# Optimization experiments

Measured on AMD Instinct MI355X. Metric: run time of the kernel, lower is better.

Reference implementation:

```python
import jax, jax.numpy as jnp
import numpy as np

K = 3
STRIDE = 1
PAD = 1
DIL = 1


def _unfold(a):
    # a: (N, C, H, W) -> patches (N, C, K*K, oH, oW), matching torch.F.unfold
    # channel-major ordering (c slowest, then kernel row, then kernel col).
    N, C, H, W = a.shape
    oH = (H + 2 * PAD - DIL * (K - 1) - 1) // STRIDE + 1
    oW = (W + 2 * PAD - DIL * (K - 1) - 1) // STRIDE + 1
    ap = jnp.pad(a, ((0, 0), (0, 0), (PAD, PAD), (PAD, PAD)))
    cols = []
    for i in range(K):
        for j in range(K):
            cols.append(ap[:, :,
                           i * DIL: i * DIL + (oH - 1) * STRIDE + 1: STRIDE,
                           j * DIL: j * DIL + (oW - 1) * STRIDE + 1: STRIDE])
    return jnp.stack(cols, axis=2)  # (N, C, K*K, oH, oW)


def setup_inputs() -> dict:
    key = jax.random.key(0)
    k1, k2, k3, k4, k5 = jax.random.split(key, 5)
    N, C, O, H, W = 4, 128, 256, 128, 128
    x = jax.random.normal(k1, (N, C, H, W), dtype=jnp.float32)
    depth = jax.random.uniform(k2, (N, 1, H, W), dtype=jnp.float32)
    camera_params = jax.random.normal(k3, (N, 4), dtype=jnp.float32)
    weight = jax.random.normal(k4, (O, C, K, K), dtype=jnp.float32) * 0.05
    bias = jax.random.normal(k5, (O,), dtype=jnp.float32) * 0.05
    return {"x": x, "depth": depth, "camera_params": camera_params,
            "weight": weight, "bias": bias}


def reference(x, depth, camera_params, weight, bias):
    # camera_params is accepted but unused, mirroring the torch module.
    O, C = weight.shape[0], weight.shape[1]
    xp = _unfold(x)        # (N, C, kk, oH, oW)
    dp = _unfold(depth)    # (N, 1, kk, oH, oW)
    w = weight.reshape(O, C, K * K)
    # depth-modulated im2col GEMM: sum_{c,p} w[o,c,p] * x_patch * d_patch
    out = jnp.einsum('ocp,ncpxy->noxy', w, xp * dp)
    return out + bias[None, :, None, None]
```

## Files before the change

kernel.cpp:

```cpp
#include <hip/hip_runtime.h>
#include <stdint.h>


#define C_IN 128
#define O_OUT 256
#define HW 128
#define NB 4
#define PADW 130

#define XD_ELEMS ((size_t)NB * PADW * PADW * C_IN)
#define XD_BYTES (XD_ELEMS * 2)
#define WT_ELEMS ((size_t)O_OUT * C_IN * 9)
#define WT_BYTES (WT_ELEMS * 2)

typedef __attribute__((ext_vector_type(8))) short short8;
typedef __attribute__((ext_vector_type(4))) float f32x4;
typedef __attribute__((ext_vector_type(4))) unsigned uint4v;

__device__ __forceinline__ unsigned f2bf_bits(float f) {
  unsigned u = __builtin_bit_cast(unsigned, f);
  return (u + 0x7fffu + ((u >> 16) & 1u)) >> 16;
}

__device__ __forceinline__ void async_load16(const void* g, void* l) {
  __builtin_amdgcn_global_load_lds(
      (__attribute__((address_space(1))) void*)g,
      (__attribute__((address_space(3))) void*)l, 16, 0, 0);
}

__global__ __launch_bounds__(256) void prep_xd(const float* __restrict__ x,
                                               const float* __restrict__ depth,
                                               short* __restrict__ xd) {
  __shared__ short s[128 * 130];

  const int R = blockIdx.x;
  if (R >= NB * HW) {
    const int n = R - NB * HW;
    uint4v* base0 = (uint4v*)(xd + (size_t)n * PADW * PADW * C_IN);
    uint4v* base1 = (uint4v*)(xd + ((size_t)n * PADW + (PADW - 1)) * PADW * C_IN);
    const uint4v z = {0u, 0u, 0u, 0u};
    const int per_row = PADW * C_IN * 2 / 16;
    for (int i = threadIdx.x; i < per_row; i += 256) {
      base0[i] = z;
      base1[i] = z;
    }
    return;
  }

  const int n = R >> 7, y = R & 127;
  const int tid = threadIdx.x;
  const int lane = tid & 63;
  const int wave = tid >> 6;

  {
    unsigned* row = (unsigned*)(xd + ((size_t)(n * PADW + y + 1) * PADW) * C_IN);
    if (tid < 64) row[tid] = 0u;
    else if (tid < 128) row[(size_t)(PADW - 1) * 64 + (tid - 64)] = 0u;
  }

  typedef __attribute__((ext_vector_type(2))) float f32x2;
  const f32x2 d2 = *(const f32x2*)(depth + ((size_t)n * HW + y) * HW + 2 * lane);
  const float* xrow = x + (((size_t)n * C_IN) * HW + y) * HW + 2 * lane;
#pragma unroll 8
  for (int ci = 0; ci < 32; ++ci) {
    const int c = ci * 4 + wave;
    const f32x2 v = *(const f32x2*)(xrow + (size_t)c * HW * HW);
    s[(2 * lane) * 130 + c] = (short)f2bf_bits(v.x * d2.x);
    s[(2 * lane + 1) * 130 + c] = (short)f2bf_bits(v.y * d2.y);
  }
  __syncthreads();

  unsigned* orow = (unsigned*)(xd + ((size_t)(n * PADW + y + 1) * PADW + 1) * C_IN);
#pragma unroll 8
  for (int i = 0; i < 32; ++i) {
    const int flat = tid + i * 256;
    const int px = flat >> 6, cp = flat & 63;
    orow[flat] = ((const unsigned*)s)[px * 65 + cp];
  }
}

__global__ void prep_wt(const float* __restrict__ w, short* __restrict__ wt) {
  const int gid = blockIdx.x * 256 + threadIdx.x;
  if (gid >= (int)WT_ELEMS) return;
  const int c = gid & 127;
  const int tap = (gid >> 7) % 9;
  const int o = gid / (9 * 128);
  wt[gid] = (short)f2bf_bits(w[((size_t)o * C_IN + c) * 9 + tap]);
}

__global__ __launch_bounds__(256, 2) void conv_mfma(
    const short* __restrict__ xd, const short* __restrict__ wt,
    const float* __restrict__ bias, float* __restrict__ out) {
  __shared__ short lds[24576];

  const int tid = threadIdx.x;
  const int bx = blockIdx.x;
  const int n = bx >> 6;
  const int y = (bx & 63) << 1;
  const int o0 = blockIdx.y << 7;
  const int lane = tid & 63;
  const int wave = tid >> 6;
  const int wm = wave & 1, wn = wave >> 1;
  const int ln = lane & 15, q = lane >> 4;

  const int row0 = tid >> 2;
  const int part = tid & 3;

  const short* wg0 = wt + (size_t)(o0 + row0) * 1152 + part * 8;
  const short* wg1 = wg0 + (size_t)64 * 1152;
  const short* xh0 = xd + ((size_t)(n * PADW + y) * PADW + row0) * C_IN + part * 8;
  const short* xh1 = xh0 + (size_t)PADW * C_IN;

  f32x4 acc[4][8] = {};

  auto stage = [&](int kt) {
    const int tap = kt >> 2;
    const int cc = kt & 3;
    const int ti = tap / 3;
    const int tj = tap - ti * 3;
    const int wo = kt << 5;
    const int xo = (ti * PADW + tj) * C_IN + (cc << 5);
    short* lb = lds + ((kt & 1) ? 12288 : 0) + tid * 8;
    async_load16(wg0 + wo, lb);
    async_load16(wg1 + wo, lb + 2048);
    async_load16(xh0 + xo, lb + 4096);
    async_load16(xh0 + 64 * C_IN + xo, lb + 6144);
    async_load16(xh1 + xo, lb + 8192);
    async_load16(xh1 + 64 * C_IN + xo, lb + 10240);
  };

  stage(0);

#pragma unroll 4
  for (int kt = 0; kt < 36; ++kt) {
    __syncthreads();

    if (kt + 1 < 36) stage(kt + 1);

    const short* Ws = lds + ((kt & 1) ? 12288 : 0);
    const short* Xs = Ws + 4096;

    short8 a[4], b[8];
#pragma unroll
    for (int t = 0; t < 4; ++t)
      a[t] = *(const short8*)(Ws + (((wm << 6) + (t << 4) + ln) << 5) + (q << 3));
#pragma unroll
    for (int u = 0; u < 8; ++u)
      b[u] = *(const short8*)(Xs + (((wn << 7) + (u << 4) + ln) << 5) + (q << 3));
#pragma unroll
    for (int t = 0; t < 4; ++t)
#pragma unroll
      for (int u = 0; u < 8; ++u)
        acc[t][u] =
            __builtin_amdgcn_mfma_f32_16x16x32_bf16(a[t], b[u], acc[t][u], 0, 0, 0);
  }

#pragma unroll
  for (int t = 0; t < 4; ++t) {
    const int ob = o0 + (wm << 6) + (t << 4) + (q << 2);
#pragma unroll
    for (int u = 0; u < 8; ++u) {
      const int xcol = (u << 4) + ln;
      const int yrow = y + wn;
#pragma unroll
      for (int r = 0; r < 4; ++r) {
        const int o = ob + r;
        out[(((size_t)n * O_OUT + o) * HW + yrow) * HW + xcol] =
            acc[t][u][r] + bias[o];
      }
    }
  }
}

__global__ void conv_naive(const float* __restrict__ x,
                           const float* __restrict__ depth,
                           const float* __restrict__ w,
                           const float* __restrict__ bias,
                           float* __restrict__ out) {
  const int gid = blockIdx.x * 256 + threadIdx.x;
  if (gid >= NB * O_OUT * HW * HW) return;
  const int xc = gid & 127;
  const int y = (gid >> 7) & 127;
  const int o = (gid >> 14) & 255;
  const int n = gid >> 22;
  float s = bias[o];
  for (int c = 0; c < C_IN; ++c)
    for (int i = 0; i < 3; ++i) {
      const int yy = y + i - 1;
      if (yy < 0 || yy >= HW) continue;
      for (int j = 0; j < 3; ++j) {
        const int xx = xc + j - 1;
        if (xx < 0 || xx >= HW) continue;
        s += w[((o * C_IN + c) * 3 + i) * 3 + j] *
             x[(((size_t)n * C_IN + c) * HW + yy) * HW + xx] *
             depth[((size_t)n * HW + yy) * HW + xx];
      }
    }
  out[gid] = s;
}

extern "C" void kernel_launch(void* const* d_in, const int* in_sizes, int n_in,
                              void* d_out, int out_size, void* d_ws, size_t ws_size,
                              hipStream_t stream) {
  const float* x = (const float*)d_in[0];
  const float* depth = (const float*)d_in[1];
  const float* weight = (const float*)d_in[3];
  const float* bias = (const float*)d_in[4];
  float* out = (float*)d_out;

  const size_t need = XD_BYTES + WT_BYTES;
  if (ws_size < need) {
    conv_naive<<<(NB * O_OUT * HW * HW + 255) / 256, 256, 0, stream>>>(
        x, depth, weight, bias, out);
    return;
  }

  short* xd = (short*)d_ws;
  short* wt = (short*)((char*)d_ws + XD_BYTES);

  prep_xd<<<NB * HW + NB, 256, 0, stream>>>(x, depth, xd);
  prep_wt<<<(int)((WT_ELEMS + 255) / 256), 256, 0, stream>>>(weight, wt);
  conv_mfma<<<dim3(NB * HW / 2, 2), 256, 0, stream>>>(xd, wt, bias, out);
}
```

Measured before the change: 139.9 us.

## Fuse prep kernels, use prefetch-depth-two for activations, repack LDS transpose

Merges the weight conversion into the activation prep kernel so one launch replaces two. The LDS transpose in prep now writes packed 32-bit pairs along channel-major rows and reassembles pairs on readout, which changes the bank-conflict pattern. The conv kernel splits staging so weights stay double-buffered while activations get a triple buffer and are prefetched two K-steps ahead, growing LDS from 48KB to 64KB per block. The extra LDS could cut how many blocks fit per CU.

```diff
diff --git a/kernel.cpp b/kernel.cpp
--- a/kernel.cpp
+++ b/kernel.cpp
@@ -15,6 +15,7 @@
 
 typedef __attribute__((ext_vector_type(8))) short short8;
 typedef __attribute__((ext_vector_type(4))) float f32x4;
+typedef __attribute__((ext_vector_type(2))) float f32x2;
 typedef __attribute__((ext_vector_type(4))) unsigned uint4v;
 
 __device__ __forceinline__ unsigned f2bf_bits(float f) {
@@ -28,12 +29,25 @@
       (__attribute__((address_space(3))) void*)l, 16, 0, 0);
 }
 
-__global__ __launch_bounds__(256) void prep_xd(const float* __restrict__ x,
-                                               const float* __restrict__ depth,
-                                               short* __restrict__ xd) {
-  __shared__ short s[128 * 130];
-
+__global__ __launch_bounds__(256) void prep_all(const float* __restrict__ x,
+                                                const float* __restrict__ depth,
+                                                const float* __restrict__ w,
+                                                short* __restrict__ xd,
+                                                short* __restrict__ wt) {
   const int R = blockIdx.x;
+
+  if (R >= NB * HW + NB) {
+    int gid = (R - (NB * HW + NB)) * 4608 + threadIdx.x;
+#pragma unroll
+    for (int i = 0; i < 18; ++i, gid += 256) {
+      const int c = gid & 127;
+      const int tap = (gid >> 7) % 9;
+      const int o = gid / 1152;
+      wt[gid] = (short)f2bf_bits(w[((size_t)o * C_IN + c) * 9 + tap]);
+    }
+    return;
+  }
+
   if (R >= NB * HW) {
     const int n = R - NB * HW;
     uint4v* base0 = (uint4v*)(xd + (size_t)n * PADW * PADW * C_IN);
@@ -47,6 +61,8 @@
     return;
   }
 
+  __shared__ short s[C_IN * PADW];
+
   const int n = R >> 7, y = R & 127;
   const int tid = threadIdx.x;
   const int lane = tid & 63;
@@ -58,40 +74,33 @@
     else if (tid < 128) row[(size_t)(PADW - 1) * 64 + (tid - 64)] = 0u;
   }
 
-  typedef __attribute__((ext_vector_type(2))) float f32x2;
   const f32x2 d2 = *(const f32x2*)(depth + ((size_t)n * HW + y) * HW + 2 * lane);
   const float* xrow = x + (((size_t)n * C_IN) * HW + y) * HW + 2 * lane;
+  unsigned* s32 = (unsigned*)s;
 #pragma unroll 8
   for (int ci = 0; ci < 32; ++ci) {
     const int c = ci * 4 + wave;
     const f32x2 v = *(const f32x2*)(xrow + (size_t)c * HW * HW);
-    s[(2 * lane) * 130 + c] = (short)f2bf_bits(v.x * d2.x);
-    s[(2 * lane + 1) * 130 + c] = (short)f2bf_bits(v.y * d2.y);
+    s32[c * 65 + lane] = f2bf_bits(v.x * d2.x) | (f2bf_bits(v.y * d2.y) << 16);
   }
   __syncthreads();
 
+  const unsigned short* s16 = (const unsigned short*)s;
   unsigned* orow = (unsigned*)(xd + ((size_t)(n * PADW + y + 1) * PADW + 1) * C_IN);
 #pragma unroll 8
   for (int i = 0; i < 32; ++i) {
     const int flat = tid + i * 256;
     const int px = flat >> 6, cp = flat & 63;
-    orow[flat] = ((const unsigned*)s)[px * 65 + cp];
-  }
-}
-
-__global__ void prep_wt(const float* __restrict__ w, short* __restrict__ wt) {
-  const int gid = blockIdx.x * 256 + threadIdx.x;
-  if (gid >= (int)WT_ELEMS) return;
-  const int c = gid & 127;
-  const int tap = (gid >> 7) % 9;
-  const int o = gid / (9 * 128);
-  wt[gid] = (short)f2bf_bits(w[((size_t)o * C_IN + c) * 9 + tap]);
+    const unsigned lo = s16[(2 * cp) * PADW + px];
+    const unsigned hi = s16[(2 * cp + 1) * PADW + px];
+    orow[flat] = lo | (hi << 16);
+  }
 }
 
 __global__ __launch_bounds__(256, 2) void conv_mfma(
     const short* __restrict__ xd, const short* __restrict__ wt,
     const float* __restrict__ bias, float* __restrict__ out) {
-  __shared__ short lds[24576];
+  __shared__ short lds[32768];
 
   const int tid = threadIdx.x;
   const int bx = blockIdx.x;
@@ -113,32 +122,38 @@
 
   f32x4 acc[4][8] = {};
 
-  auto stage = [&](int kt) {
+  auto stageW = [&](int kt) {
+    short* lb = lds + ((kt & 1) << 12) + tid * 8;
+    const int wo = kt << 5;
+    async_load16(wg0 + wo, lb);
+    async_load16(wg1 + wo, lb + 2048);
+  };
+  auto stageX = [&](int kt) {
     const int tap = kt >> 2;
     const int cc = kt & 3;
     const int ti = tap / 3;
     const int tj = tap - ti * 3;
-    const int wo = kt << 5;
     const int xo = (ti * PADW + tj) * C_IN + (cc << 5);
-    short* lb = lds + ((kt & 1) ? 12288 : 0) + tid * 8;
-    async_load16(wg0 + wo, lb);
-    async_load16(wg1 + wo, lb + 2048);
-    async_load16(xh0 + xo, lb + 4096);
-    async_load16(xh0 + 64 * C_IN + xo, lb + 6144);
-    async_load16(xh1 + xo, lb + 8192);
-    async_load16(xh1 + 64 * C_IN + xo, lb + 10240);
+    short* lb = lds + 8192 + (kt % 3) * 8192 + tid * 8;
+    async_load16(xh0 + xo, lb);
+    async_load16(xh0 + 64 * C_IN + xo, lb + 2048);
+    async_load16(xh1 + xo, lb + 4096);
+    async_load16(xh1 + 64 * C_IN + xo, lb + 6144);
   };
 
-  stage(0);
-
-#pragma unroll 4
+  stageW(0);
+  stageX(0);
+  stageX(1);
+
+#pragma unroll 6
   for (int kt = 0; kt < 36; ++kt) {
     __syncthreads();
 
-    if (kt + 1 < 36) stage(kt + 1);
-
-    const short* Ws = lds + ((kt & 1) ? 12288 : 0);
-    const short* Xs = Ws + 4096;
+    if (kt + 1 < 36) stageW(kt + 1);
+    if (kt + 2 < 36) stageX(kt + 2);
+
+    const short* Ws = lds + ((kt & 1) << 12);
+    const short* Xs = lds + 8192 + (kt % 3) * 8192;
 
     short8 a[4], b[8];
 #pragma unroll
@@ -218,7 +233,6 @@
   short* xd = (short*)d_ws;
   short* wt = (short*)((char*)d_ws + XD_BYTES);
 
-  prep_xd<<<NB * HW + NB, 256, 0, stream>>>(x, depth, xd);
-  prep_wt<<<(int)((WT_ELEMS + 255) / 256), 256, 0, stream>>>(weight, wt);
+  prep_all<<<NB * HW + NB + 64, 256, 0, stream>>>(x, depth, weight, xd, wt);
   conv_mfma<<<dim3(NB * HW / 2, 2), 256, 0, stream>>>(xd, wt, bias, out);
 }
```

After: 136.8 us. 2.2% less time.
